# Performance work log

Hardware: AMD Instinct MI355X
Metric: run time of the kernel (lower is better)

## Reference

```python
import jax, jax.numpy as jnp
import numpy as np

C = 256
C8 = C // 8  # query/key channels
B, T, W, H = 4, 8, 32, 32


def setup_inputs() -> dict:
    key = jax.random.key(0)
    ks = jax.random.split(key, 8)
    s = 0.05
    return {
        "x": jax.random.normal(ks[0], (B, C, T, W, H), dtype=jnp.float32),
        "wq": jax.random.normal(ks[1], (C8, C), dtype=jnp.float32) * s,
        "bq": jax.random.normal(ks[2], (C8,), dtype=jnp.float32) * s,
        "wk": jax.random.normal(ks[3], (C8, C), dtype=jnp.float32) * s,
        "bk": jax.random.normal(ks[4], (C8,), dtype=jnp.float32) * s,
        "wv": jax.random.normal(ks[5], (C, C), dtype=jnp.float32) * s,
        "bv": jax.random.normal(ks[6], (C,), dtype=jnp.float32) * s,
        "gamma": jax.random.normal(ks[7], (1,), dtype=jnp.float32),
    }


def reference(x, wq, bq, wk, bk, wv, bv, gamma):
    b, c, t, w, h = x.shape
    n = w * h
    # Faithful to torch: x.view(-1, c, w, h) is a row-major reinterpretation
    xr = jnp.reshape(x, (-1, c, n))  # (m, C, N), m = B*T
    # 1x1 convs == per-pixel linear projections
    q = jnp.einsum("oc,mcn->mno", wq, xr) + bq            # (m, N, C8)
    k = jnp.einsum("oc,mcn->mon", wk, xr) + bk[:, None]   # (m, C8, N)
    v = jnp.einsum("oc,mcn->mon", wv, xr) + bv[:, None]   # (m, C, N)
    energy = jnp.einsum("mic,mcj->mij", q, k)             # (m, N, N), unscaled
    attention = jax.nn.softmax(energy, axis=-1)
    out = jnp.einsum("mcn,mnj->mcj", v, attention)        # V @ A (as in torch code)
    out = jnp.reshape(out, (b, c, t, w, h))
    return gamma * out + x
```

## Files before the change

kernel.cpp:

```cpp
#include <hip/hip_runtime.h>

#define MB    32
#define CCH   256
#define QCH   32
#define NPIX  1024
#define SLICE (CCH * NPIX)
#define L2E   1.44269504088896340736f
#define SHIFT 32.0f

typedef __bf16          bf16x8 __attribute__((ext_vector_type(8)));
typedef __bf16          bf16x4 __attribute__((ext_vector_type(4)));
typedef float           f32x4  __attribute__((ext_vector_type(4)));
typedef unsigned int    u32x4  __attribute__((ext_vector_type(4)));
typedef unsigned short  u16x4  __attribute__((ext_vector_type(4)));

__device__ __forceinline__ unsigned short f2bf(float f) {
    unsigned int u = __builtin_bit_cast(unsigned int, f);
    u += 0x7FFFu + ((u >> 16) & 1u);
    return (unsigned short)(u >> 16);
}
__device__ __forceinline__ u16x4 cvt4(float a, float b, float c, float d) {
    bf16x4 v = { (__bf16)a, (__bf16)b, (__bf16)c, (__bf16)d };
    return __builtin_bit_cast(u16x4, v);
}
__device__ __forceinline__ float bf2f(unsigned short u) {
    unsigned int v = (unsigned int)u << 16;
    return __builtin_bit_cast(float, v);
}
__device__ __forceinline__ bf16x8 ldfrag(const unsigned short* p) {
    u32x4 u = *(const u32x4*)p;
    return __builtin_bit_cast(bf16x8, u);
}

#define WB_OFF  0u
#define QT_OFF  262144u
#define KT_OFF  2359296u
#define V_OFF   4456448u
#define A2F_OFF 21233664u
#define PU_OFF  21364736u
#define WS_NEED 88473600u

__global__ __launch_bounds__(256) void k_prep_w(
    const float* __restrict__ wq, const float* __restrict__ wk,
    const float* __restrict__ wv, unsigned short* __restrict__ Wb)
{
    int i4 = (blockIdx.x * 256 + threadIdx.x) * 4;
    int o = i4 >> 8, c = i4 & 255;
    const float* src = (o < 32) ? wq + (size_t)o * CCH + c
                     : (o < 64) ? wk + (size_t)(o - 32) * CCH + c
                                : wv + (size_t)(o - 64) * CCH + c;
    float4 v = *(const float4*)src;
    *(u16x4*)(Wb + i4) = cvt4(v.x, v.y, v.z, v.w);
}

__global__ __launch_bounds__(256) void k_proj(
    const float* __restrict__ x, const unsigned short* __restrict__ Wb,
    const float* __restrict__ bq, const float* __restrict__ bk,
    const float* __restrict__ bv,
    unsigned short* __restrict__ Qt, unsigned short* __restrict__ Kt,
    unsigned short* __restrict__ V)
{
    __shared__ unsigned short Xs[64 * 268];

    const int t = threadIdx.x, lane = t & 63, w = t >> 6;
    const int lj = lane & 15, q = lane >> 4;
    const int n0 = blockIdx.x * 64;
    const int mi = blockIdx.y;
    const float* xp = x + (size_t)mi * SLICE;

#pragma unroll
    for (int r = 0; r < 8; ++r) {
        int job = t + r * 256;
        int cp = job >> 4;
        int seg = job & 15;
        float4 va = *(const float4*)(xp + (size_t)(2 * cp) * NPIX + n0 + seg * 4);
        float4 vb = *(const float4*)(xp + (size_t)(2 * cp + 1) * NPIX + n0 + seg * 4);
        u16x4 da = cvt4(va.x, va.y, va.z, va.w);
        u16x4 db = cvt4(vb.x, vb.y, vb.z, vb.w);
#pragma unroll
        for (int e = 0; e < 4; ++e) {
            unsigned pk = (unsigned)da[e] | ((unsigned)db[e] << 16);
            *(unsigned*)&Xs[(seg * 4 + e) * 268 + 2 * cp] = pk;
        }
    }
    __syncthreads();

    f32x4 acc[5][4];
#pragma unroll
    for (int i = 0; i < 5; ++i)
#pragma unroll
        for (int b = 0; b < 4; ++b) acc[i][b] = (f32x4){0.f, 0.f, 0.f, 0.f};

    const unsigned short* wbase = Wb + (size_t)(w * 16 + lj) * CCH + q * 8;
    const unsigned short* xbase = &Xs[lj * 268 + q * 8];

#pragma unroll 2
    for (int kc = 0; kc < CCH; kc += 32) {
        bf16x8 a[5];
#pragma unroll
        for (int i = 0; i < 5; ++i)
            a[i] = ldfrag(wbase + (size_t)i * 64 * CCH + kc);
        bf16x8 xb[4];
#pragma unroll
        for (int b = 0; b < 4; ++b)
            xb[b] = ldfrag(xbase + b * 16 * 268 + kc);
#pragma unroll
        for (int i = 0; i < 5; ++i)
#pragma unroll
            for (int b = 0; b < 4; ++b)
                acc[i][b] = __builtin_amdgcn_mfma_f32_16x16x32_bf16(a[i], xb[b], acc[i][b], 0, 0, 0);
    }

#pragma unroll
    for (int i = 0; i < 5; ++i) {
        const int o16 = (w + 4 * i) * 16;
        const int ob = o16 + 4 * q;
        if (o16 < 32) {
            unsigned short* Qp = Qt + (size_t)mi * NPIX * QCH;
            float b0 = bq[ob], b1 = bq[ob + 1], b2 = bq[ob + 2], b3 = bq[ob + 3];
#pragma unroll
            for (int b = 0; b < 4; ++b) {
                int n = n0 + b * 16 + lj;
                *(u16x4*)(Qp + (size_t)n * QCH + ob) =
                    cvt4((acc[i][b][0] + b0) * L2E, (acc[i][b][1] + b1) * L2E,
                         (acc[i][b][2] + b2) * L2E, (acc[i][b][3] + b3) * L2E);
            }
        } else if (o16 < 64) {
            unsigned short* Kp = Kt + (size_t)mi * NPIX * QCH;
            int o2 = ob - 32;
            float b0 = bk[o2], b1 = bk[o2 + 1], b2 = bk[o2 + 2], b3 = bk[o2 + 3];
#pragma unroll
            for (int b = 0; b < 4; ++b) {
                int n = n0 + b * 16 + lj;
                *(u16x4*)(Kp + (size_t)n * QCH + o2) =
                    cvt4(acc[i][b][0] + b0, acc[i][b][1] + b1,
                         acc[i][b][2] + b2, acc[i][b][3] + b3);
            }
        } else {
            unsigned short* Vw = V + (size_t)mi * SLICE;
            const int c16 = (o16 - 64) >> 4;
            const int n05 = n0 >> 5;
            const int cb = (o16 - 64) + 4 * q;
            float bb[4] = { bv[cb], bv[cb + 1], bv[cb + 2], bv[cb + 3] };
            const int ni = lj & 7;
#pragma unroll
            for (int b = 0; b < 4; ++b) {
                int n5 = n05 + (b >> 1);
                int fl = ((2 * b + (lj >> 3)) & 3) * 16 + 4 * q;
                size_t base = ((size_t)(c16 * 32 + n5) * 64 + fl) * 8 + ni;
#pragma unroll
                for (int r = 0; r < 4; ++r)
                    Vw[base + (size_t)r * 8] = f2bf(acc[i][b][r] + bb[r]);
            }
        }
    }
}

__global__ __launch_bounds__(256) void k_stats_pu(
    const unsigned short* __restrict__ Qt, const unsigned short* __restrict__ Kt,
    unsigned short* __restrict__ V, unsigned short* __restrict__ Pu)
{
    __shared__ unsigned short Ps[4][32][36];
    __shared__ float rs[128];

    const int t = threadIdx.x, lane = t & 63, w = t >> 6;
    const int lj = lane & 15, q = lane >> 4;
    const int n0b = blockIdx.x * 128;
    const int nw = n0b + w * 32;
    const int mi = blockIdx.y;
    const unsigned short* Qp = Qt + (size_t)mi * NPIX * QCH;
    const unsigned short* Kp = Kt + (size_t)mi * NPIX * QCH;
    unsigned short* Pup = Pu + (size_t)mi * NPIX * NPIX;

    bf16x8 qa[2];
#pragma unroll
    for (int h = 0; h < 2; ++h)
        qa[h] = ldfrag(Qp + (size_t)(nw + h * 16 + lj) * QCH + q * 8);

    float s[2][4];
#pragma unroll
    for (int h = 0; h < 2; ++h)
#pragma unroll
        for (int r = 0; r < 4; ++r) s[h][r] = 0.f;

#pragma unroll 2
    for (int jc = 0; jc < NPIX; jc += 32) {
#pragma unroll
        for (int f = 0; f < 2; ++f) {
            bf16x8 kb = ldfrag(Kp + (size_t)(jc + f * 16 + lj) * QCH + q * 8);
#pragma unroll
            for (int h = 0; h < 2; ++h) {
                f32x4 z = (f32x4){0.f, 0.f, 0.f, 0.f};
                f32x4 e = __builtin_amdgcn_mfma_f32_16x16x32_bf16(qa[h], kb, z, 0, 0, 0);
                float p0 = exp2f(e[0] - SHIFT), p1 = exp2f(e[1] - SHIFT);
                float p2 = exp2f(e[2] - SHIFT), p3 = exp2f(e[3] - SHIFT);
                s[h][0] += p0; s[h][1] += p1; s[h][2] += p2; s[h][3] += p3;
                *(u16x4*)&Ps[w][f * 16 + lj][h * 16 + 4 * q] = cvt4(p0, p1, p2, p3);
            }
        }
#pragma unroll
        for (int f = 0; f < 2; ++f) {
            u32x4 bfrag = *(const u32x4*)&Ps[w][f * 16 + lj][q * 8];
            *(u32x4*)(Pup + ((size_t)((jc >> 4) + f) * 32 + (nw >> 5)) * 512 + lane * 8) = bfrag;
        }
    }

#pragma unroll
    for (int msk = 1; msk <= 8; msk <<= 1)
#pragma unroll
        for (int h = 0; h < 2; ++h)
#pragma unroll
            for (int r = 0; r < 4; ++r) s[h][r] += __shfl_xor(s[h][r], msk, 64);
    if (lj == 0) {
#pragma unroll
        for (int h = 0; h < 2; ++h)
#pragma unroll
            for (int r = 0; r < 4; ++r)
                rs[w * 32 + h * 16 + 4 * q + r] = 1.0f / s[h][r];
    }
    __syncthreads();

    unsigned short* Vp = V + (size_t)mi * SLICE;
    const int n5b = n0b >> 5;
#pragma unroll
    for (int r = 0; r < 16; ++r) {
        int job = t + r * 256;
        int fr = job >> 6, ln = job & 63;
        size_t base = ((size_t)((fr >> 2) * 32 + n5b + (fr & 3)) * 64 + ln) * 8;
        u16x4 lo = *(const u16x4*)(Vp + base);
        u16x4 hi = *(const u16x4*)(Vp + base + 4);
        const float* rp = &rs[(fr & 3) * 32 + (ln >> 4) * 8];
        u16x4 nlo = cvt4(bf2f(lo[0]) * rp[0], bf2f(lo[1]) * rp[1],
                         bf2f(lo[2]) * rp[2], bf2f(lo[3]) * rp[3]);
        u16x4 nhi = cvt4(bf2f(hi[0]) * rp[4], bf2f(hi[1]) * rp[5],
                         bf2f(hi[2]) * rp[6], bf2f(hi[3]) * rp[7]);
        *(u16x4*)(Vp + base) = nlo;
        *(u16x4*)(Vp + base + 4) = nhi;
    }
}

__global__ __launch_bounds__(256) void k_gemm_out(
    const float* __restrict__ x, const float* __restrict__ gamma,
    const unsigned short* __restrict__ Vf, const unsigned short* __restrict__ Pu,
    float* __restrict__ out)
{
    __shared__ unsigned short Vs[2][8 * 512];

    const int b = blockIdx.x;
    const int mi  = (b & 7) | ((b >> 7) << 3);
    const int sub = (b >> 3) & 15;
    const int j0  = (sub & 7) * 128;
    const int cb  = sub >> 3;

    const int t = threadIdx.x, lane = t & 63, w = t >> 6;
    const int lj = lane & 15, q = lane >> 4;
    const int jw = j0 + w * 32;

    const unsigned short* Vp  = Vf + (size_t)mi * SLICE;
    const unsigned short* Pup = Pu + (size_t)mi * NPIX * NPIX
                              + ((size_t)(jw >> 4) * 32) * 512 + lane * 8;

    const int ctl = t >> 5, ln0 = (t & 31) * 2;
    const unsigned short* vsrc0 = Vp + ((size_t)(cb * 8 + ctl) * 32) * 512 + ln0 * 8;

    f32x4 acc[8][2];
#pragma unroll
    for (int ci = 0; ci < 8; ++ci)
#pragma unroll
        for (int f = 0; f < 2; ++f) acc[ci][f] = (f32x4){0.f, 0.f, 0.f, 0.f};

    {
        u32x4 d0 = *(const u32x4*)vsrc0;
        u32x4 d1 = *(const u32x4*)(vsrc0 + 8);
        *(u32x4*)&Vs[0][ctl * 512 + ln0 * 8] = d0;
        *(u32x4*)&Vs[0][ctl * 512 + ln0 * 8 + 8] = d1;
    }
    bf16x8 pf[2];
#pragma unroll
    for (int f = 0; f < 2; ++f) pf[f] = ldfrag(Pup + f * 16384);
    __syncthreads();

    int p = 0;
    for (int nc = 0; nc < NPIX; nc += 32, p ^= 1) {
        const int nn = (nc + 32) & (NPIX - 1);
        const unsigned short* vsrc = vsrc0 + (size_t)(nn >> 5) * 512;
        u32x4 nv0 = *(const u32x4*)vsrc;
        u32x4 nv1 = *(const u32x4*)(vsrc + 8);
        bf16x8 pf_n[2];
#pragma unroll
        for (int f = 0; f < 2; ++f)
            pf_n[f] = ldfrag(Pup + f * 16384 + (size_t)(nn >> 5) * 512);

#pragma unroll
        for (int ci = 0; ci < 8; ++ci) {
            bf16x8 vfr = ldfrag(&Vs[p][ci * 512 + lane * 8]);
#pragma unroll
            for (int f = 0; f < 2; ++f)
                acc[ci][f] = __builtin_amdgcn_mfma_f32_16x16x32_bf16(vfr, pf[f], acc[ci][f], 0, 0, 0);
        }

        *(u32x4*)&Vs[p ^ 1][ctl * 512 + ln0 * 8] = nv0;
        *(u32x4*)&Vs[p ^ 1][ctl * 512 + ln0 * 8 + 8] = nv1;
        __syncthreads();
        pf[0] = pf_n[0]; pf[1] = pf_n[1];
    }

    const float g = gamma[0];
    const size_t obase = (size_t)mi * SLICE;
#pragma unroll
    for (int ci = 0; ci < 8; ++ci) {
#pragma unroll
        for (int f = 0; f < 2; ++f) {
#pragma unroll
            for (int r = 0; r < 4; ++r) {
                int c = cb * 128 + ci * 16 + 4 * q + r;
                int j = jw + f * 16 + lj;
                size_t off = obase + (size_t)c * NPIX + j;
                out[off] = g * acc[ci][f][r] + x[off];
            }
        }
    }
}

__global__ __launch_bounds__(256) void k_stats(
    const unsigned short* __restrict__ Qt, const unsigned short* __restrict__ Kt,
    float* __restrict__ a2f)
{
    const int t = threadIdx.x, lane = t & 63, w = t >> 6;
    const int lj = lane & 15, q = lane >> 4;
    const int n16 = blockIdx.x * 64 + w * 16;
    const int mi = blockIdx.y;
    const unsigned short* Qp = Qt + (size_t)mi * NPIX * QCH;
    const unsigned short* Kp = Kt + (size_t)mi * NPIX * QCH;

    bf16x8 qa = ldfrag(Qp + (size_t)(n16 + lj) * QCH + q * 8);

    float s[4] = { 0.f, 0.f, 0.f, 0.f };
#pragma unroll 8
    for (int jc = 0; jc < NPIX; jc += 16) {
        bf16x8 kb = ldfrag(Kp + (size_t)(jc + lj) * QCH + q * 8);
        f32x4 z = (f32x4){0.f, 0.f, 0.f, 0.f};
        f32x4 e = __builtin_amdgcn_mfma_f32_16x16x32_bf16(qa, kb, z, 0, 0, 0);
#pragma unroll
        for (int r = 0; r < 4; ++r) s[r] += exp2f(e[r] - SHIFT);
    }
#pragma unroll
    for (int msk = 1; msk <= 8; msk <<= 1)
#pragma unroll
        for (int r = 0; r < 4; ++r) s[r] += __shfl_xor(s[r], msk, 64);
    if (lj == 0) {
        float* apo = a2f + (size_t)mi * NPIX;
#pragma unroll
        for (int r = 0; r < 4; ++r)
            apo[n16 + 4 * q + r] = SHIFT + log2f(s[r]);
    }
}

__global__ __launch_bounds__(256) void k_attn_out(
    const float* __restrict__ x, const float* __restrict__ gamma,
    const unsigned short* __restrict__ Qt, const unsigned short* __restrict__ Kt,
    const unsigned short* __restrict__ Vf, const float* __restrict__ a2f,
    float* __restrict__ out)
{
    __shared__ unsigned short Vs[2][8 * 512];
    __shared__ unsigned short Ps[4][32][36];

    const int b = blockIdx.x;
    const int mi  = (b & 7) | ((b >> 7) << 3);
    const int sub = (b >> 3) & 15;
    const int j0  = (sub & 7) * 128;
    const int cb  = sub >> 3;

    const int t = threadIdx.x, lane = t & 63, w = t >> 6;
    const int lj = lane & 15, q = lane >> 4;
    const int jw = j0 + w * 32;

    const unsigned short* Qp = Qt + (size_t)mi * NPIX * QCH;
    const unsigned short* Kp = Kt + (size_t)mi * NPIX * QCH;
    const unsigned short* Vp = Vf + (size_t)mi * SLICE;
    const float* ap = a2f + (size_t)mi * NPIX;

    bf16x8 kb[2];
#pragma unroll
    for (int sj = 0; sj < 2; ++sj)
        kb[sj] = ldfrag(Kp + (size_t)(jw + sj * 16 + lj) * QCH + q * 8);

    const int ctl = t >> 5, ln0 = (t & 31) * 2;
    const unsigned short* vsrc0 = Vp + ((size_t)(cb * 8 + ctl) * 32) * 512 + ln0 * 8;

    f32x4 acc[8][2];
#pragma unroll
    for (int ci = 0; ci < 8; ++ci)
#pragma unroll
        for (int ji = 0; ji < 2; ++ji) acc[ci][ji] = (f32x4){0.f, 0.f, 0.f, 0.f};

    {
        u32x4 d0 = *(const u32x4*)vsrc0;
        u32x4 d1 = *(const u32x4*)(vsrc0 + 8);
        *(u32x4*)&Vs[0][ctl * 512 + ln0 * 8] = d0;
        *(u32x4*)&Vs[0][ctl * 512 + ln0 * 8 + 8] = d1;
    }
    bf16x8 qa_n[2];
    f32x4  a4_n[2];
#pragma unroll
    for (int sn = 0; sn < 2; ++sn) {
        qa_n[sn] = ldfrag(Qp + (size_t)(sn * 16 + lj) * QCH + q * 8);
        a4_n[sn] = *(const f32x4*)(ap + sn * 16 + 4 * q);
    }
    __syncthreads();

    int p = 0;
    for (int nc = 0; nc < NPIX; nc += 32, p ^= 1) {
        const int nn = (nc + 32) & (NPIX - 1);
        const unsigned short* vsrc = vsrc0 + (size_t)(nn >> 5) * 512;
        u32x4 nv0 = *(const u32x4*)vsrc;
        u32x4 nv1 = *(const u32x4*)(vsrc + 8);

        bf16x8 qa0 = qa_n[0], qa1 = qa_n[1];
        f32x4 a40 = a4_n[0], a41 = a4_n[1];
#pragma unroll
        for (int sj = 0; sj < 2; ++sj) {
            f32x4 z = (f32x4){0.f, 0.f, 0.f, 0.f};
            f32x4 e0 = __builtin_amdgcn_mfma_f32_16x16x32_bf16(qa0, kb[sj], z, 0, 0, 0);
            f32x4 e1 = __builtin_amdgcn_mfma_f32_16x16x32_bf16(qa1, kb[sj], z, 0, 0, 0);
            *(u16x4*)&Ps[w][sj * 16 + lj][4 * q] =
                cvt4(exp2f(e0[0] - a40[0]), exp2f(e0[1] - a40[1]),
                     exp2f(e0[2] - a40[2]), exp2f(e0[3] - a40[3]));
            *(u16x4*)&Ps[w][sj * 16 + lj][16 + 4 * q] =
                cvt4(exp2f(e1[0] - a41[0]), exp2f(e1[1] - a41[1]),
                     exp2f(e1[2] - a41[2]), exp2f(e1[3] - a41[3]));
        }
#pragma unroll
        for (int sn = 0; sn < 2; ++sn) {
            qa_n[sn] = ldfrag(Qp + (size_t)(nn + sn * 16 + lj) * QCH + q * 8);
            a4_n[sn] = *(const f32x4*)(ap + nn + sn * 16 + 4 * q);
        }

        bf16x8 pf[2];
#pragma unroll
        for (int ji = 0; ji < 2; ++ji)
            pf[ji] = ldfrag(&Ps[w][ji * 16 + lj][q * 8]);
#pragma unroll
        for (int ci = 0; ci < 8; ++ci) {
            bf16x8 vfr = ldfrag(&Vs[p][ci * 512 + lane * 8]);
#pragma unroll
            for (int ji = 0; ji < 2; ++ji)
                acc[ci][ji] = __builtin_amdgcn_mfma_f32_16x16x32_bf16(vfr, pf[ji], acc[ci][ji], 0, 0, 0);
        }

        *(u32x4*)&Vs[p ^ 1][ctl * 512 + ln0 * 8] = nv0;
        *(u32x4*)&Vs[p ^ 1][ctl * 512 + ln0 * 8 + 8] = nv1;
        __syncthreads();
    }

    const float g = gamma[0];
    const size_t obase = (size_t)mi * SLICE;
#pragma unroll
    for (int ci = 0; ci < 8; ++ci) {
#pragma unroll
        for (int ji = 0; ji < 2; ++ji) {
#pragma unroll
            for (int r = 0; r < 4; ++r) {
                int c = cb * 128 + ci * 16 + 4 * q + r;
                int j = jw + ji * 16 + lj;
                size_t off = obase + (size_t)c * NPIX + j;
                out[off] = g * acc[ci][ji][r] + x[off];
            }
        }
    }
}

extern "C" void kernel_launch(void* const* d_in, const int* in_sizes, int n_in,
                              void* d_out, int out_size, void* d_ws, size_t ws_size,
                              hipStream_t stream)
{
    const float* x     = (const float*)d_in[0];
    const float* wq    = (const float*)d_in[1];
    const float* bq    = (const float*)d_in[2];
    const float* wk    = (const float*)d_in[3];
    const float* bk    = (const float*)d_in[4];
    const float* wv    = (const float*)d_in[5];
    const float* bv    = (const float*)d_in[6];
    const float* gamma = (const float*)d_in[7];
    float* out = (float*)d_out;

    char* wsb = (char*)d_ws;
    unsigned short* Wb = (unsigned short*)(wsb + WB_OFF);
    unsigned short* Qt = (unsigned short*)(wsb + QT_OFF);
    unsigned short* Kt = (unsigned short*)(wsb + KT_OFF);
    unsigned short* V  = (unsigned short*)(wsb + V_OFF);
    float*          a2 = (float*)(wsb + A2F_OFF);
    unsigned short* Pu = (unsigned short*)(wsb + PU_OFF);

    k_prep_w<<<80, 256, 0, stream>>>(wq, wk, wv, Wb);
    k_proj<<<dim3(NPIX / 64, MB), 256, 0, stream>>>(x, Wb, bq, bk, bv, Qt, Kt, V);

    if (ws_size >= (size_t)WS_NEED) {
        k_stats_pu<<<dim3(NPIX / 128, MB), 256, 0, stream>>>(Qt, Kt, V, Pu);
        k_gemm_out<<<512, 256, 0, stream>>>(x, gamma, V, Pu, out);
    } else {
        k_stats<<<dim3(NPIX / 64, MB), 256, 0, stream>>>(Qt, Kt, a2);
        k_attn_out<<<512, 256, 0, stream>>>(x, gamma, Qt, Kt, V, a2, out);
    }
}
```

Before: 169.0 us.

## Split stats and P materialization into separate kernels; deepen gemm K-step

```diff
diff --git a/kernel.cpp b/kernel.cpp
--- a/kernel.cpp
+++ b/kernel.cpp
@@ -156,172 +156,6 @@
     }
 }
 
-__global__ __launch_bounds__(256) void k_stats_pu(
-    const unsigned short* __restrict__ Qt, const unsigned short* __restrict__ Kt,
-    unsigned short* __restrict__ V, unsigned short* __restrict__ Pu)
-{
-    __shared__ unsigned short Ps[4][32][36];
-    __shared__ float rs[128];
-
-    const int t = threadIdx.x, lane = t & 63, w = t >> 6;
-    const int lj = lane & 15, q = lane >> 4;
-    const int n0b = blockIdx.x * 128;
-    const int nw = n0b + w * 32;
-    const int mi = blockIdx.y;
-    const unsigned short* Qp = Qt + (size_t)mi * NPIX * QCH;
-    const unsigned short* Kp = Kt + (size_t)mi * NPIX * QCH;
-    unsigned short* Pup = Pu + (size_t)mi * NPIX * NPIX;
-
-    bf16x8 qa[2];
-#pragma unroll
-    for (int h = 0; h < 2; ++h)
-        qa[h] = ldfrag(Qp + (size_t)(nw + h * 16 + lj) * QCH + q * 8);
-
-    float s[2][4];
-#pragma unroll
-    for (int h = 0; h < 2; ++h)
-#pragma unroll
-        for (int r = 0; r < 4; ++r) s[h][r] = 0.f;
-
-#pragma unroll 2
-    for (int jc = 0; jc < NPIX; jc += 32) {
-#pragma unroll
-        for (int f = 0; f < 2; ++f) {
-            bf16x8 kb = ldfrag(Kp + (size_t)(jc + f * 16 + lj) * QCH + q * 8);
-#pragma unroll
-            for (int h = 0; h < 2; ++h) {
-                f32x4 z = (f32x4){0.f, 0.f, 0.f, 0.f};
-                f32x4 e = __builtin_amdgcn_mfma_f32_16x16x32_bf16(qa[h], kb, z, 0, 0, 0);
-                float p0 = exp2f(e[0] - SHIFT), p1 = exp2f(e[1] - SHIFT);
-                float p2 = exp2f(e[2] - SHIFT), p3 = exp2f(e[3] - SHIFT);
-                s[h][0] += p0; s[h][1] += p1; s[h][2] += p2; s[h][3] += p3;
-                *(u16x4*)&Ps[w][f * 16 + lj][h * 16 + 4 * q] = cvt4(p0, p1, p2, p3);
-            }
-        }
-#pragma unroll
-        for (int f = 0; f < 2; ++f) {
-            u32x4 bfrag = *(const u32x4*)&Ps[w][f * 16 + lj][q * 8];
-            *(u32x4*)(Pup + ((size_t)((jc >> 4) + f) * 32 + (nw >> 5)) * 512 + lane * 8) = bfrag;
-        }
-    }
-
-#pragma unroll
-    for (int msk = 1; msk <= 8; msk <<= 1)
-#pragma unroll
-        for (int h = 0; h < 2; ++h)
-#pragma unroll
-            for (int r = 0; r < 4; ++r) s[h][r] += __shfl_xor(s[h][r], msk, 64);
-    if (lj == 0) {
-#pragma unroll
-        for (int h = 0; h < 2; ++h)
-#pragma unroll
-            for (int r = 0; r < 4; ++r)
-                rs[w * 32 + h * 16 + 4 * q + r] = 1.0f / s[h][r];
-    }
-    __syncthreads();
-
-    unsigned short* Vp = V + (size_t)mi * SLICE;
-    const int n5b = n0b >> 5;
-#pragma unroll
-    for (int r = 0; r < 16; ++r) {
-        int job = t + r * 256;
-        int fr = job >> 6, ln = job & 63;
-        size_t base = ((size_t)((fr >> 2) * 32 + n5b + (fr & 3)) * 64 + ln) * 8;
-        u16x4 lo = *(const u16x4*)(Vp + base);
-        u16x4 hi = *(const u16x4*)(Vp + base + 4);
-        const float* rp = &rs[(fr & 3) * 32 + (ln >> 4) * 8];
-        u16x4 nlo = cvt4(bf2f(lo[0]) * rp[0], bf2f(lo[1]) * rp[1],
-                         bf2f(lo[2]) * rp[2], bf2f(lo[3]) * rp[3]);
-        u16x4 nhi = cvt4(bf2f(hi[0]) * rp[4], bf2f(hi[1]) * rp[5],
-                         bf2f(hi[2]) * rp[6], bf2f(hi[3]) * rp[7]);
-        *(u16x4*)(Vp + base) = nlo;
-        *(u16x4*)(Vp + base + 4) = nhi;
-    }
-}
-
-__global__ __launch_bounds__(256) void k_gemm_out(
-    const float* __restrict__ x, const float* __restrict__ gamma,
-    const unsigned short* __restrict__ Vf, const unsigned short* __restrict__ Pu,
-    float* __restrict__ out)
-{
-    __shared__ unsigned short Vs[2][8 * 512];
-
-    const int b = blockIdx.x;
-    const int mi  = (b & 7) | ((b >> 7) << 3);
-    const int sub = (b >> 3) & 15;
-    const int j0  = (sub & 7) * 128;
-    const int cb  = sub >> 3;
-
-    const int t = threadIdx.x, lane = t & 63, w = t >> 6;
-    const int lj = lane & 15, q = lane >> 4;
-    const int jw = j0 + w * 32;
-
-    const unsigned short* Vp  = Vf + (size_t)mi * SLICE;
-    const unsigned short* Pup = Pu + (size_t)mi * NPIX * NPIX
-                              + ((size_t)(jw >> 4) * 32) * 512 + lane * 8;
-
-    const int ctl = t >> 5, ln0 = (t & 31) * 2;
-    const unsigned short* vsrc0 = Vp + ((size_t)(cb * 8 + ctl) * 32) * 512 + ln0 * 8;
-
-    f32x4 acc[8][2];
-#pragma unroll
-    for (int ci = 0; ci < 8; ++ci)
-#pragma unroll
-        for (int f = 0; f < 2; ++f) acc[ci][f] = (f32x4){0.f, 0.f, 0.f, 0.f};
-
-    {
-        u32x4 d0 = *(const u32x4*)vsrc0;
-        u32x4 d1 = *(const u32x4*)(vsrc0 + 8);
-        *(u32x4*)&Vs[0][ctl * 512 + ln0 * 8] = d0;
-        *(u32x4*)&Vs[0][ctl * 512 + ln0 * 8 + 8] = d1;
-    }
-    bf16x8 pf[2];
-#pragma unroll
-    for (int f = 0; f < 2; ++f) pf[f] = ldfrag(Pup + f * 16384);
-    __syncthreads();
-
-    int p = 0;
-    for (int nc = 0; nc < NPIX; nc += 32, p ^= 1) {
-        const int nn = (nc + 32) & (NPIX - 1);
-        const unsigned short* vsrc = vsrc0 + (size_t)(nn >> 5) * 512;
-        u32x4 nv0 = *(const u32x4*)vsrc;
-        u32x4 nv1 = *(const u32x4*)(vsrc + 8);
-        bf16x8 pf_n[2];
-#pragma unroll
-        for (int f = 0; f < 2; ++f)
-            pf_n[f] = ldfrag(Pup + f * 16384 + (size_t)(nn >> 5) * 512);
-
-#pragma unroll
-        for (int ci = 0; ci < 8; ++ci) {
-            bf16x8 vfr = ldfrag(&Vs[p][ci * 512 + lane * 8]);
-#pragma unroll
-            for (int f = 0; f < 2; ++f)
-                acc[ci][f] = __builtin_amdgcn_mfma_f32_16x16x32_bf16(vfr, pf[f], acc[ci][f], 0, 0, 0);
-        }
-
-        *(u32x4*)&Vs[p ^ 1][ctl * 512 + ln0 * 8] = nv0;
-        *(u32x4*)&Vs[p ^ 1][ctl * 512 + ln0 * 8 + 8] = nv1;
-        __syncthreads();
-        pf[0] = pf_n[0]; pf[1] = pf_n[1];
-    }
-
-    const float g = gamma[0];
-    const size_t obase = (size_t)mi * SLICE;
-#pragma unroll
-    for (int ci = 0; ci < 8; ++ci) {
-#pragma unroll
-        for (int f = 0; f < 2; ++f) {
-#pragma unroll
-            for (int r = 0; r < 4; ++r) {
-                int c = cb * 128 + ci * 16 + 4 * q + r;
-                int j = jw + f * 16 + lj;
-                size_t off = obase + (size_t)c * NPIX + j;
-                out[off] = g * acc[ci][f][r] + x[off];
-            }
-        }
-    }
-}
-
 __global__ __launch_bounds__(256) void k_stats(
     const unsigned short* __restrict__ Qt, const unsigned short* __restrict__ Kt,
     float* __restrict__ a2f)
@@ -353,6 +187,158 @@
 #pragma unroll
         for (int r = 0; r < 4; ++r)
             apo[n16 + 4 * q + r] = SHIFT + log2f(s[r]);
+    }
+}
+
+__global__ __launch_bounds__(256) void k_pu(
+    const unsigned short* __restrict__ Qt, const unsigned short* __restrict__ Kt,
+    const float* __restrict__ a2f, unsigned short* __restrict__ Pu)
+{
+    __shared__ unsigned short Ps[4][32][36];
+
+    const int t = threadIdx.x, lane = t & 63, w = t >> 6;
+    const int lj = lane & 15, q = lane >> 4;
+    const int nb = blockIdx.x >> 1;
+    const int jh = blockIdx.x & 1;
+    const int nw = nb * 128 + w * 32;
+    const int mi = blockIdx.y;
+    const unsigned short* Qp = Qt + (size_t)mi * NPIX * QCH;
+    const unsigned short* Kp = Kt + (size_t)mi * NPIX * QCH;
+    const float* ap = a2f + (size_t)mi * NPIX;
+    unsigned short* Pup = Pu + (size_t)mi * NPIX * NPIX;
+
+    bf16x8 qa[2];
+    f32x4  a4[2];
+#pragma unroll
+    for (int h = 0; h < 2; ++h) {
+        qa[h] = ldfrag(Qp + (size_t)(nw + h * 16 + lj) * QCH + q * 8);
+        a4[h] = *(const f32x4*)(ap + nw + h * 16 + 4 * q);
+    }
+
+    const int jbeg = jh * 512;
+#pragma unroll 2
+    for (int jc = jbeg; jc < jbeg + 512; jc += 32) {
+#pragma unroll
+        for (int f = 0; f < 2; ++f) {
+            bf16x8 kb = ldfrag(Kp + (size_t)(jc + f * 16 + lj) * QCH + q * 8);
+#pragma unroll
+            for (int h = 0; h < 2; ++h) {
+                f32x4 z = (f32x4){0.f, 0.f, 0.f, 0.f};
+                f32x4 e = __builtin_amdgcn_mfma_f32_16x16x32_bf16(qa[h], kb, z, 0, 0, 0);
+                *(u16x4*)&Ps[w][f * 16 + lj][h * 16 + 4 * q] =
+                    cvt4(exp2f(e[0] - a4[h][0]), exp2f(e[1] - a4[h][1]),
+                         exp2f(e[2] - a4[h][2]), exp2f(e[3] - a4[h][3]));
+            }
+        }
+#pragma unroll
+        for (int f = 0; f < 2; ++f) {
+            u32x4 bfrag = *(const u32x4*)&Ps[w][f * 16 + lj][q * 8];
+            *(u32x4*)(Pup + ((size_t)((jc >> 4) + f) * 32 + (nw >> 5)) * 512 + lane * 8) = bfrag;
+        }
+    }
+}
+
+__global__ __launch_bounds__(256) void k_gemm_out(
+    const float* __restrict__ x, const float* __restrict__ gamma,
+    const unsigned short* __restrict__ Vf, const unsigned short* __restrict__ Pu,
+    float* __restrict__ out)
+{
+    __shared__ unsigned short Vs[2][2 * 8 * 512];
+
+    const int b = blockIdx.x;
+    const int mi  = (b & 7) | ((b >> 7) << 3);
+    const int sub = (b >> 3) & 15;
+    const int j0  = (sub & 7) * 128;
+    const int cb  = sub >> 3;
+
+    const int t = threadIdx.x, lane = t & 63, w = t >> 6;
+    const int lj = lane & 15, q = lane >> 4;
+    const int jw = j0 + w * 32;
+
+    const unsigned short* Vp  = Vf + (size_t)mi * SLICE;
+    const unsigned short* Pup = Pu + (size_t)mi * NPIX * NPIX
+                              + ((size_t)(jw >> 4) * 32) * 512 + lane * 8;
+
+    const int ctl = t >> 5, ln0 = (t & 31) * 2;
+    const unsigned short* vsrc0 = Vp + ((size_t)(cb * 8 + ctl) * 32) * 512 + ln0 * 8;
+
+    f32x4 acc[8][2];
+#pragma unroll
+    for (int ci = 0; ci < 8; ++ci)
+#pragma unroll
+        for (int f = 0; f < 2; ++f) acc[ci][f] = (f32x4){0.f, 0.f, 0.f, 0.f};
+
+    {
+        u32x4 a0 = *(const u32x4*)(vsrc0);
+        u32x4 a1 = *(const u32x4*)(vsrc0 + 8);
+        u32x4 b0 = *(const u32x4*)(vsrc0 + 512);
+        u32x4 b1 = *(const u32x4*)(vsrc0 + 520);
+        *(u32x4*)&Vs[0][ctl * 512 + ln0 * 8]            = a0;
+        *(u32x4*)&Vs[0][ctl * 512 + ln0 * 8 + 8]        = a1;
+        *(u32x4*)&Vs[0][4096 + ctl * 512 + ln0 * 8]     = b0;
+        *(u32x4*)&Vs[0][4096 + ctl * 512 + ln0 * 8 + 8] = b1;
+    }
+    bf16x8 pf[2][2];
+#pragma unroll
+    for (int h = 0; h < 2; ++h)
+#pragma unroll
+        for (int f = 0; f < 2; ++f)
+            pf[h][f] = ldfrag(Pup + f * 16384 + (size_t)h * 512);
+    __syncthreads();
+
+    int p = 0;
+    for (int nc = 0; nc < NPIX; nc += 64, p ^= 1) {
+        const int nn = (nc + 64) & (NPIX - 1);
+        const unsigned short* vsrc = vsrc0 + (size_t)(nn >> 5) * 512;
+        u32x4 nv0 = *(const u32x4*)vsrc;
+        u32x4 nv1 = *(const u32x4*)(vsrc + 8);
+        u32x4 nv2 = *(const u32x4*)(vsrc + 512);
+        u32x4 nv3 = *(const u32x4*)(vsrc + 520);
+        bf16x8 pf_n[2][2];
+#pragma unroll
+        for (int h = 0; h < 2; ++h)
+#pragma unroll
+            for (int f = 0; f < 2; ++f)
+                pf_n[h][f] = ldfrag(Pup + f * 16384 + ((size_t)(nn >> 5) + h) * 512);
+
+        __builtin_amdgcn_s_setprio(1);
+#pragma unroll
+        for (int h = 0; h < 2; ++h) {
+#pragma unroll
+            for (int ci = 0; ci < 8; ++ci) {
+                bf16x8 vfr = ldfrag(&Vs[p][h * 4096 + ci * 512 + lane * 8]);
+#pragma unroll
+                for (int f = 0; f < 2; ++f)
+                    acc[ci][f] = __builtin_amdgcn_mfma_f32_16x16x32_bf16(vfr, pf[h][f], acc[ci][f], 0, 0, 0);
+            }
+        }
+        __builtin_amdgcn_s_setprio(0);
+
+        *(u32x4*)&Vs[p ^ 1][ctl * 512 + ln0 * 8]            = nv0;
+        *(u32x4*)&Vs[p ^ 1][ctl * 512 + ln0 * 8 + 8]        = nv1;
+        *(u32x4*)&Vs[p ^ 1][4096 + ctl * 512 + ln0 * 8]     = nv2;
+        *(u32x4*)&Vs[p ^ 1][4096 + ctl * 512 + ln0 * 8 + 8] = nv3;
+        __syncthreads();
+#pragma unroll
+        for (int h = 0; h < 2; ++h)
+#pragma unroll
+            for (int f = 0; f < 2; ++f) pf[h][f] = pf_n[h][f];
+    }
+
+    const float g = gamma[0];
+    const size_t obase = (size_t)mi * SLICE;
+#pragma unroll
+    for (int ci = 0; ci < 8; ++ci) {
+#pragma unroll
+        for (int f = 0; f < 2; ++f) {
+#pragma unroll
+            for (int r = 0; r < 4; ++r) {
+                int c = cb * 128 + ci * 16 + 4 * q + r;
+                int j = jw + f * 16 + lj;
+                size_t off = obase + (size_t)c * NPIX + j;
+                out[off] = g * acc[ci][f][r] + x[off];
+            }
+        }
     }
 }
 
@@ -494,12 +480,12 @@
 
     k_prep_w<<<80, 256, 0, stream>>>(wq, wk, wv, Wb);
     k_proj<<<dim3(NPIX / 64, MB), 256, 0, stream>>>(x, Wb, bq, bk, bv, Qt, Kt, V);
+    k_stats<<<dim3(NPIX / 64, MB), 256, 0, stream>>>(Qt, Kt, a2);
 
     if (ws_size >= (size_t)WS_NEED) {
-        k_stats_pu<<<dim3(NPIX / 128, MB), 256, 0, stream>>>(Qt, Kt, V, Pu);
+        k_pu<<<dim3(16, MB), 256, 0, stream>>>(Qt, Kt, a2, Pu);
         k_gemm_out<<<512, 256, 0, stream>>>(x, gamma, V, Pu, out);
     } else {
-        k_stats<<<dim3(NPIX / 64, MB), 256, 0, stream>>>(Qt, Kt, a2);
         k_attn_out<<<512, 256, 0, stream>>>(x, gamma, Qt, Kt, V, a2, out);
     }
 }
```

Measured after the change: 172.8 us. 2.3% more time.
